# Kernel tuning notes

Hardware: AMD Instinct MI355X
Metric: run time of the kernel (lower is better)

The kernel has to match this reference:

```python
import jax, jax.numpy as jnp
import numpy as np

ROPE_BASE = 10000.0


def _rope(x):
    # Faithful to the torch module: positions indexed by x.shape[2],
    # which after split_heads is the HEADS axis. x: [B, S, H, D]
    B, S, H, D = x.shape
    theta = 1.0 / (ROPE_BASE ** (jnp.arange(0, D, 2, dtype=x.dtype) / D))  # [D/2]
    pos = jnp.arange(H, dtype=x.dtype)[:, None]  # [H, 1]
    ang = pos * theta  # [H, D/2], broadcasts against [B, S, H, D/2]
    sin, cos = jnp.sin(ang), jnp.cos(ang)
    xe, xo = x[..., 0::2], x[..., 1::2]
    re = xe * cos - xo * sin
    ro = xe * sin + xo * cos
    # interleave back: even slots <- re, odd slots <- ro
    return jnp.stack([re, ro], axis=-1).reshape(B, S, H, D)


def setup_inputs() -> dict:
    key = jax.random.key(0)
    k0, k1, k2, k3 = jax.random.split(key, 4)
    B, S, Dm = 8, 2048, 2048
    scale = 1.0 / np.sqrt(Dm)
    return {
        "x": jax.random.normal(k0, (B, S, Dm), dtype=jnp.float32),
        "Wq": jax.random.normal(k1, (Dm, Dm), dtype=jnp.float32) * scale,
        "Wk": jax.random.normal(k2, (Dm, Dm), dtype=jnp.float32) * scale,
        "Wv": jax.random.normal(k3, (Dm, Dm), dtype=jnp.float32) * scale,
        "st_pos": 0,
    }


def reference(x, Wq, Wk, Wv, st_pos):
    B, S, Dm = x.shape
    H = 16
    D = Dm // H  # head_dim = 128
    q = jnp.einsum("bsd,df->bsf", x, Wq).reshape(B, S, H, D)
    k = jnp.einsum("bsd,df->bsf", x, Wk).reshape(B, S, H, D)
    v = jnp.einsum("bsd,df->bsf", x, Wv).reshape(B, S, H, D)
    q = _rope(q)
    k = _rope(k)
    return q, k, v
```

## Files before the change

kernel.cpp:

```cpp
#include <hip/hip_runtime.h>
#include <hip/hip_bf16.h>
#include <stdint.h>


typedef __attribute__((ext_vector_type(8))) short short8;
typedef __attribute__((ext_vector_type(4))) float f32x4;

__device__ __forceinline__ unsigned short f2bf(float f) {
  __bf16 h = (__bf16)f;
  return __builtin_bit_cast(unsigned short, h);
}

__device__ __forceinline__ void gload_lds16(const void* g, void* l) {
  __builtin_amdgcn_global_load_lds((const __attribute__((address_space(1))) void*)g,
                                   (__attribute__((address_space(3))) void*)l,
                                   16, 0, 0);
}


__global__ __launch_bounds__(256) void convert_x(const float* __restrict__ X,
                                                 unsigned short* __restrict__ Xb,
                                                 int n8) {
  const int stride = gridDim.x * blockDim.x;
  for (int i = blockIdx.x * blockDim.x + threadIdx.x; i < n8; i += stride) {
    const float4 v0 = ((const float4*)X)[(size_t)i * 2 + 0];
    const float4 v1 = ((const float4*)X)[(size_t)i * 2 + 1];
    uint4 w;
    w.x = (uint32_t)f2bf(v0.x) | ((uint32_t)f2bf(v0.y) << 16);
    w.y = (uint32_t)f2bf(v0.z) | ((uint32_t)f2bf(v0.w) << 16);
    w.z = (uint32_t)f2bf(v1.x) | ((uint32_t)f2bf(v1.y) << 16);
    w.w = (uint32_t)f2bf(v1.z) | ((uint32_t)f2bf(v1.w) << 16);
    ((uint4*)Xb)[i] = w;
  }
}

__global__ __launch_bounds__(256) void transpose_cvt(const float* __restrict__ W,
                                                     unsigned short* __restrict__ WT) {
  __shared__ unsigned short tile[64][65];
  const int bx = blockIdx.x * 64;
  const int by = blockIdx.y * 64;
  const int t  = threadIdx.x;
  const int tr = t >> 4;
  const int tc = (t & 15) * 4;
#pragma unroll
  for (int i = 0; i < 4; ++i) {
    const int r = tr + i * 16;
    const float4 v = *(const float4*)&W[(size_t)(by + r) * 2048 + bx + tc];
    tile[r][tc + 0] = f2bf(v.x);
    tile[r][tc + 1] = f2bf(v.y);
    tile[r][tc + 2] = f2bf(v.z);
    tile[r][tc + 3] = f2bf(v.w);
  }
  __syncthreads();
#pragma unroll
  for (int i = 0; i < 4; ++i) {
    const int a = tr + i * 16;
    ushort4 o;
    o.x = tile[tc + 0][a];
    o.y = tile[tc + 1][a];
    o.z = tile[tc + 2][a];
    o.w = tile[tc + 3][a];
    *(ushort4*)&WT[(size_t)(bx + a) * 2048 + by + tc] = o;
  }
}


__global__ __launch_bounds__(512, 2) void qkv_fused10(const unsigned short* __restrict__ Xb,
                                                      const unsigned short* __restrict__ WT,
                                                      float* __restrict__ Out) {
  extern __shared__ char smem[];

  const int wg  = blockIdx.x;
  const int swz = (wg & 7) * 192 + (wg >> 3);
  const int mb  = swz / 24, nb = swz % 24;
  const int m0  = mb * 256, n0 = nb * 256;

  const int tid  = threadIdx.x;
  const int wave = tid >> 6, lane = tid & 63;
  const int l15  = lane & 15, lg = lane >> 4;
  const int wm   = (wave >> 2) * 128;
  const int wn   = (wave & 3) * 64;
  const int s0   = ((lg ^ (l15 & 7)) << 4);

  const unsigned short* Xp = Xb + (size_t)m0 * 2048;
  const unsigned short* Wp = WT + (size_t)n0 * 2048;

  const int srow  = tid >> 3;
  const int sslot = tid & 7;

  f32x4 acc[8][4] = {};

#define GLD_A(TP1, H)                                                         \
  do {                                                                        \
    char* dst_ = smem + (((TP1) & 1) << 16) + ((H) << 14);                    \
    _Pragma("unroll") for (int i_ = 0; i_ < 2; ++i_) {                        \
      const int row_ = (H) * 128 + i_ * 64 + srow;                            \
      gload_lds16(Xp + (size_t)row_ * 2048 + (TP1) * 64 +                     \
                      ((sslot ^ (row_ & 7)) << 3),                            \
                  dst_ + i_ * 8192 + tid * 16);                               \
    }                                                                         \
  } while (0)

#define GLD_B(TP2, H)                                                         \
  do {                                                                        \
    char* dst_ = smem + (((TP2) & 1) << 16) + 32768 + ((H) << 14);            \
    _Pragma("unroll") for (int i_ = 0; i_ < 2; ++i_) {                        \
      const int row_ = (H) * 128 + i_ * 64 + srow;                            \
      gload_lds16(Wp + (size_t)row_ * 2048 + (TP2) * 64 +                     \
                      ((sslot ^ (row_ & 7)) << 3),                            \
                  dst_ + i_ * 8192 + tid * 16);                               \
    }                                                                         \
  } while (0)

#define LDA4(MH, KS)                                                          \
  _Pragma("unroll") for (int mi_ = 0; mi_ < 4; ++mi_)                         \
      af[mi_] = *(const short8*)(Ab + ((wm + (MH) * 64 + mi_ * 16 + l15) << 7)\
                                  + (s0 ^ ((KS) << 6)));

#define PHASE_SYNC                                                            \
  __builtin_amdgcn_s_barrier();                                               \
  asm volatile("s_waitcnt lgkmcnt(0)" ::: "memory");                          \
  __builtin_amdgcn_sched_barrier(0);

#define MFMA16(MH, KS)                                                        \
  do {                                                                        \
    __builtin_amdgcn_s_setprio(1);                                            \
    _Pragma("unroll") for (int mi_ = 0; mi_ < 4; ++mi_)                       \
      _Pragma("unroll") for (int ni_ = 0; ni_ < 4; ++ni_)                     \
        asm("v_mfma_f32_16x16x32_bf16 %0, %1, %2, %0"                         \
            : "+v"(acc[(MH) * 4 + mi_][ni_])                                  \
            : "v"(af[mi_]), "v"(bfr[ni_][KS]));                               \
    __builtin_amdgcn_s_setprio(0);                                            \
  } while (0)

  GLD_A(0, 0); GLD_A(0, 1);
  GLD_B(0, 0); GLD_B(0, 1);
  GLD_B(1, 0); GLD_B(1, 1);
  asm volatile("s_waitcnt vmcnt(4)" ::: "memory");
  __builtin_amdgcn_s_barrier();

  for (int t = 0; t < 32; ++t) {
    const char* Ab = smem + ((t & 1) << 16);
    const char* Bb = Ab + 32768;
    short8 bfr[4][2], af[4];

#pragma unroll
    for (int ni_ = 0; ni_ < 4; ++ni_) {
      const char* p_ = Bb + ((wn + ni_ * 16 + l15) << 7);
      bfr[ni_][0] = *(const short8*)(p_ + s0);
      bfr[ni_][1] = *(const short8*)(p_ + (s0 ^ 64));
    }
    LDA4(0, 0);
    if (t < 31) GLD_A(t + 1, 0);
    PHASE_SYNC;
    MFMA16(0, 0);
    __builtin_amdgcn_s_barrier();

    LDA4(1, 0);
    if (t < 31) GLD_A(t + 1, 1);
    PHASE_SYNC;
    MFMA16(1, 0);
    __builtin_amdgcn_s_barrier();

    LDA4(0, 1);
    if (t < 30) GLD_B(t + 2, 0);
    PHASE_SYNC;
    MFMA16(0, 1);
    __builtin_amdgcn_s_barrier();

    LDA4(1, 1);
    if (t < 30) GLD_B(t + 2, 1);
    PHASE_SYNC;
    MFMA16(1, 1);
    if (t == 30)     asm volatile("s_waitcnt vmcnt(0)" ::: "memory");
    else if (t < 30) asm volatile("s_waitcnt vmcnt(4)" ::: "memory");
    __builtin_amdgcn_s_barrier();
  }

#undef GLD_A
#undef GLD_B
#undef LDA4
#undef PHASE_SYNC
#undef MFMA16

#pragma unroll
  for (int ni = 0; ni < 4; ++ni) {
    const int col = n0 + wn + ni * 16 + l15;
    const int sec = col >> 11;
    const int lc  = col & 2047;
    float c = 1.0f, ssg = 0.0f;
    if (sec < 2) {
      const int h = lc >> 7;
      const int p = (lc & 127) >> 1;
      const float theta = exp2f(-(float)p * 0.20762050593046014f);
      float s;
      sincosf((float)h * theta, &s, &c);
      ssg = (l15 & 1) ? s : -s;
    }
    float* outp = Out + (size_t)sec * 33554432 + lc;
#pragma unroll
    for (int mi = 0; mi < 8; ++mi) {
      const f32x4 a = acc[mi][ni];
#pragma unroll
      for (int r = 0; r < 4; ++r) {
        const float val = a[r];
        float res = val;
        if (sec < 2) {
          const float other = __shfl_xor(val, 1);
          res = val * c + other * ssg;
        }
        __builtin_nontemporal_store(
            res, outp + (size_t)(m0 + wm + mi * 16 + lg * 4 + r) * 2048);
      }
    }
  }
}

__global__ __launch_bounds__(256) void qkv_gemm_small(const float* __restrict__ X,
                                                      const unsigned short* __restrict__ WTl,
                                                      float* __restrict__ Out,
                                                      const int do_rope) {
  __shared__ unsigned short As[128 * 64];
  __shared__ unsigned short Bs[128 * 64];
  const int t    = threadIdx.x;
  const int wave = t >> 6, lane = t & 63;
  const int l15  = lane & 15, lg = lane >> 4;
  const int wm   = (wave >> 1) * 64;
  const int wn   = (wave & 1) * 64;
  const int m0   = blockIdx.y * 128;
  const int n0   = blockIdx.x * 128;

  f32x4 acc[4][4] = {};

  for (int kt = 0; kt < 2048; kt += 64) {
#pragma unroll
    for (int i = 0; i < 8; ++i) {
      const int f = i * 256 + t;
      const int row = f >> 4, chunk = f & 15;
      const float4 v = *(const float4*)&X[(size_t)(m0 + row) * 2048 + kt + chunk * 4];
      const uint32_t lo = (uint32_t)f2bf(v.x) | ((uint32_t)f2bf(v.y) << 16);
      const uint32_t hi = (uint32_t)f2bf(v.z) | ((uint32_t)f2bf(v.w) << 16);
      const int slot = chunk >> 1;
      const int off  = row * 128 + (((slot ^ (row & 7)) << 4) | ((chunk & 1) << 3));
      uint2* p = (uint2*)((char*)As + off);
      p->x = lo; p->y = hi;
    }
#pragma unroll
    for (int i = 0; i < 4; ++i) {
      const int seg = i * 4 + wave;
      const int row = seg * 8 + (lane >> 3);
      const int ps  = lane & 7;
      const int ss  = ps ^ (row & 7);
      gload_lds16(WTl + (size_t)(n0 + row) * 2048 + kt + ss * 8,
                  (char*)Bs + seg * 1024 + lane * 16);
    }
    __syncthreads();
#pragma unroll
    for (int kk = 0; kk < 2; ++kk) {
      short8 afr[4], bfr[4];
#pragma unroll
      for (int mi = 0; mi < 4; ++mi) {
        const int row  = wm + mi * 16 + l15;
        const int slot = kk * 4 + lg;
        afr[mi] = *(const short8*)((const char*)As + row * 128 + ((slot ^ (row & 7)) << 4));
      }
#pragma unroll
      for (int ni = 0; ni < 4; ++ni) {
        const int row  = wn + ni * 16 + l15;
        const int slot = kk * 4 + lg;
        bfr[ni] = *(const short8*)((const char*)Bs + row * 128 + ((slot ^ (row & 7)) << 4));
      }
#pragma unroll
      for (int mi = 0; mi < 4; ++mi)
#pragma unroll
        for (int ni = 0; ni < 4; ++ni)
          asm("v_mfma_f32_16x16x32_bf16 %0, %1, %2, %0"
              : "+v"(acc[mi][ni])
              : "v"(afr[mi]), "v"(bfr[ni]));
    }
    __syncthreads();
  }

#pragma unroll
  for (int ni = 0; ni < 4; ++ni) {
    const int col = n0 + wn + ni * 16 + l15;
    float c = 1.0f, ssg = 0.0f;
    if (do_rope) {
      const int h = col >> 7;
      const int p = (col & 127) >> 1;
      const float theta = exp2f(-(float)p * 0.20762050593046014f);
      float s;
      sincosf((float)h * theta, &s, &c);
      ssg = (l15 & 1) ? s : -s;
    }
#pragma unroll
    for (int mi = 0; mi < 4; ++mi) {
      const f32x4 a = acc[mi][ni];
#pragma unroll
      for (int r = 0; r < 4; ++r) {
        const float val = a[r];
        float res = val;
        if (do_rope) {
          const float other = __shfl_xor(val, 1);
          res = val * c + other * ssg;
        }
        Out[(size_t)(m0 + wm + mi * 16 + lg * 4 + r) * 2048 + col] = res;
      }
    }
  }
}

extern "C" void kernel_launch(void* const* d_in, const int* in_sizes, int n_in,
                              void* d_out, int out_size, void* d_ws, size_t ws_size,
                              hipStream_t stream) {
  (void)in_sizes; (void)n_in; (void)out_size;
  const float* x  = (const float*)d_in[0];
  const float* Wq = (const float*)d_in[1];
  const float* Wk = (const float*)d_in[2];
  const float* Wv = (const float*)d_in[3];
  float* out = (float*)d_out;

  const size_t XB_ELEMS = 16384ull * 2048;
  const size_t WT_ELEMS = 6144ull * 2048;
  dim3 tb(256), tg(32, 32);

  if (ws_size >= (XB_ELEMS + WT_ELEMS) * sizeof(unsigned short)) {
    unsigned short* Xb  = (unsigned short*)d_ws;
    unsigned short* WTf = Xb + XB_ELEMS;
    convert_x<<<2048, 256, 0, stream>>>(x, Xb, (int)(XB_ELEMS / 8));
    transpose_cvt<<<tg, tb, 0, stream>>>(Wq, WTf);
    transpose_cvt<<<tg, tb, 0, stream>>>(Wk, WTf + 2048ull * 2048);
    transpose_cvt<<<tg, tb, 0, stream>>>(Wv, WTf + 2ull * 2048 * 2048);
    hipFuncSetAttribute((const void*)qkv_fused10,
                        hipFuncAttributeMaxDynamicSharedMemorySize, 131072);
    qkv_fused10<<<1536, 512, 131072, stream>>>(Xb, WTf, out);
  } else {
    unsigned short* WqT = (unsigned short*)d_ws;
    unsigned short* WkT = WqT + 2048ull * 2048;
    unsigned short* WvT = WkT + 2048ull * 2048;
    transpose_cvt<<<tg, tb, 0, stream>>>(Wq, WqT);
    transpose_cvt<<<tg, tb, 0, stream>>>(Wk, WkT);
    transpose_cvt<<<tg, tb, 0, stream>>>(Wv, WvT);
    dim3 gg(16, 128);
    qkv_gemm_small<<<gg, tb, 0, stream>>>(x, WqT, out,            1);
    qkv_gemm_small<<<gg, tb, 0, stream>>>(x, WkT, out + 33554432, 1);
    qkv_gemm_small<<<gg, tb, 0, stream>>>(x, WvT, out + 67108864, 0);
  }
}
```

Before: 445.0 us.

## Switch GEMM to 32x32x16 MFMA with fragment-ordered LDS layout and merge transposes

Result: slower. 492.1 us (+10.6%).

```diff
diff --git a/kernel.cpp b/kernel.cpp
--- a/kernel.cpp
+++ b/kernel.cpp
@@ -3,8 +3,9 @@
 #include <stdint.h>
 
 
-typedef __attribute__((ext_vector_type(8))) short short8;
-typedef __attribute__((ext_vector_type(4))) float f32x4;
+typedef __attribute__((ext_vector_type(8)))  short short8;
+typedef __attribute__((ext_vector_type(4)))  float f32x4;
+typedef __attribute__((ext_vector_type(16))) float f32x16;
 
 __device__ __forceinline__ unsigned short f2bf(float f) {
   __bf16 h = (__bf16)f;
@@ -34,9 +35,14 @@
   }
 }
 
-__global__ __launch_bounds__(256) void transpose_cvt(const float* __restrict__ W,
-                                                     unsigned short* __restrict__ WT) {
+__global__ __launch_bounds__(256) void transpose_cvt3(const float* __restrict__ W0,
+                                                      const float* __restrict__ W1,
+                                                      const float* __restrict__ W2,
+                                                      unsigned short* __restrict__ WT) {
   __shared__ unsigned short tile[64][65];
+  const int z = blockIdx.z;
+  const float* W = (z == 0) ? W0 : (z == 1) ? W1 : W2;
+  unsigned short* WTz = WT + (size_t)z * 2048 * 2048;
   const int bx = blockIdx.x * 64;
   const int by = blockIdx.y * 64;
   const int t  = threadIdx.x;
@@ -60,12 +66,12 @@
     o.y = tile[tc + 1][a];
     o.z = tile[tc + 2][a];
     o.w = tile[tc + 3][a];
-    *(ushort4*)&WT[(size_t)(bx + a) * 2048 + by + tc] = o;
-  }
-}
-
-
-__global__ __launch_bounds__(512, 2) void qkv_fused10(const unsigned short* __restrict__ Xb,
+    *(ushort4*)&WTz[(size_t)(bx + a) * 2048 + by + tc] = o;
+  }
+}
+
+
+__global__ __launch_bounds__(512, 2) void qkv_fused11(const unsigned short* __restrict__ Xb,
                                                       const unsigned short* __restrict__ WT,
                                                       float* __restrict__ Out) {
   extern __shared__ char smem[];
@@ -77,59 +83,60 @@
 
   const int tid  = threadIdx.x;
   const int wave = tid >> 6, lane = tid & 63;
-  const int l15  = lane & 15, lg = lane >> 4;
+  const int l31  = lane & 31;
   const int wm   = (wave >> 2) * 128;
   const int wn   = (wave & 3) * 64;
-  const int s0   = ((lg ^ (l15 & 7)) << 4);
+  const int am   = (wave >> 2) * 4;
+  const int bn   = (wave & 3) * 2;
 
   const unsigned short* Xp = Xb + (size_t)m0 * 2048;
   const unsigned short* Wp = WT + (size_t)n0 * 2048;
 
-  const int srow  = tid >> 3;
-  const int sslot = tid & 7;
-
-  f32x4 acc[8][4] = {};
-
-#define GLD_A(TP1, H)                                                         \
+  const int sg_rowb = ((tid >> 8) << 5) + (tid & 31);
+  const int sg_koff = ((tid >> 5) & 7) * 8;
+
+  f32x16 acc[4][2] = {};
+
+#define GLD_A(TP, P)                                                          \
   do {                                                                        \
-    char* dst_ = smem + (((TP1) & 1) << 16) + ((H) << 14);                    \
+    char* dst_ = smem + (((TP) & 1) << 16);                                   \
     _Pragma("unroll") for (int i_ = 0; i_ < 2; ++i_) {                        \
-      const int row_ = (H) * 128 + i_ * 64 + srow;                            \
-      gload_lds16(Xp + (size_t)row_ * 2048 + (TP1) * 64 +                     \
-                      ((sslot ^ (row_ & 7)) << 3),                            \
-                  dst_ + i_ * 8192 + tid * 16);                               \
+      const int ch_ = 2 * (P) + i_;                                           \
+      gload_lds16(Xp + (size_t)(ch_ * 64 + sg_rowb) * 2048 + (TP) * 64 +      \
+                      sg_koff,                                                \
+                  dst_ + ch_ * 8192 + tid * 16);                              \
     }                                                                         \
   } while (0)
 
-#define GLD_B(TP2, H)                                                         \
+#define GLD_B(TP, P)                                                          \
   do {                                                                        \
-    char* dst_ = smem + (((TP2) & 1) << 16) + 32768 + ((H) << 14);            \
+    char* dst_ = smem + (((TP) & 1) << 16) + 32768;                           \
     _Pragma("unroll") for (int i_ = 0; i_ < 2; ++i_) {                        \
-      const int row_ = (H) * 128 + i_ * 64 + srow;                            \
-      gload_lds16(Wp + (size_t)row_ * 2048 + (TP2) * 64 +                     \
-                      ((sslot ^ (row_ & 7)) << 3),                            \
-                  dst_ + i_ * 8192 + tid * 16);                               \
+      const int ch_ = 2 * (P) + i_;                                           \
+      gload_lds16(Wp + (size_t)(ch_ * 64 + sg_rowb) * 2048 + (TP) * 64 +      \
+                      sg_koff,                                                \
+                  dst_ + ch_ * 8192 + tid * 16);                              \
     }                                                                         \
   } while (0)
 
-#define LDA4(MH, KS)                                                          \
-  _Pragma("unroll") for (int mi_ = 0; mi_ < 4; ++mi_)                         \
-      af[mi_] = *(const short8*)(Ab + ((wm + (MH) * 64 + mi_ * 16 + l15) << 7)\
-                                  + (s0 ^ ((KS) << 6)));
+#define LDA4(KS)                                                              \
+  _Pragma("unroll") for (int m_ = 0; m_ < 4; ++m_)                            \
+      af[m_] = *(const short8*)(Ab + (am + m_) * 4096 + (KS) * 1024 +         \
+                                lane * 16);
 
 #define PHASE_SYNC                                                            \
   __builtin_amdgcn_s_barrier();                                               \
   asm volatile("s_waitcnt lgkmcnt(0)" ::: "memory");                          \
   __builtin_amdgcn_sched_barrier(0);
 
-#define MFMA16(MH, KS)                                                        \
+#define MFMA8(KS)                                                             \
   do {                                                                        \
     __builtin_amdgcn_s_setprio(1);                                            \
-    _Pragma("unroll") for (int mi_ = 0; mi_ < 4; ++mi_)                       \
-      _Pragma("unroll") for (int ni_ = 0; ni_ < 4; ++ni_)                     \
-        asm("v_mfma_f32_16x16x32_bf16 %0, %1, %2, %0"                         \
-            : "+v"(acc[(MH) * 4 + mi_][ni_])                                  \
-            : "v"(af[mi_]), "v"(bfr[ni_][KS]));                               \
+    _Pragma("unroll") for (int m_ = 0; m_ < 4; ++m_)                          \
+      _Pragma("unroll") for (int n_ = 0; n_ < 2; ++n_)                        \
+        asm("v_mfma_f32_32x32x16_bf16 %0, %1, %2, %0"                         \
+            : "+v"(acc[m_][n_])                                               \
+            : "v"(af[m_]), "v"(bfr[n_][KS]));                                 \
     __builtin_amdgcn_s_setprio(0);                                            \
   } while (0)
 
@@ -142,36 +149,36 @@
   for (int t = 0; t < 32; ++t) {
     const char* Ab = smem + ((t & 1) << 16);
     const char* Bb = Ab + 32768;
-    short8 bfr[4][2], af[4];
-
-#pragma unroll
-    for (int ni_ = 0; ni_ < 4; ++ni_) {
-      const char* p_ = Bb + ((wn + ni_ * 16 + l15) << 7);
-      bfr[ni_][0] = *(const short8*)(p_ + s0);
-      bfr[ni_][1] = *(const short8*)(p_ + (s0 ^ 64));
-    }
-    LDA4(0, 0);
+    short8 bfr[2][4], af[4];
+
+#pragma unroll
+    for (int n_ = 0; n_ < 2; ++n_)
+#pragma unroll
+      for (int ks_ = 0; ks_ < 4; ++ks_)
+        bfr[n_][ks_] = *(const short8*)(Bb + (bn + n_) * 4096 + ks_ * 1024 +
+                                        lane * 16);
+    LDA4(0);
     if (t < 31) GLD_A(t + 1, 0);
     PHASE_SYNC;
-    MFMA16(0, 0);
+    MFMA8(0);
     __builtin_amdgcn_s_barrier();
 
-    LDA4(1, 0);
+    LDA4(1);
     if (t < 31) GLD_A(t + 1, 1);
     PHASE_SYNC;
-    MFMA16(1, 0);
+    MFMA8(1);
     __builtin_amdgcn_s_barrier();
 
-    LDA4(0, 1);
+    LDA4(2);
     if (t < 30) GLD_B(t + 2, 0);
     PHASE_SYNC;
-    MFMA16(0, 1);
+    MFMA8(2);
     __builtin_amdgcn_s_barrier();
 
-    LDA4(1, 1);
+    LDA4(3);
     if (t < 30) GLD_B(t + 2, 1);
     PHASE_SYNC;
-    MFMA16(1, 1);
+    MFMA8(3);
     if (t == 30)     asm volatile("s_waitcnt vmcnt(0)" ::: "memory");
     else if (t < 30) asm volatile("s_waitcnt vmcnt(4)" ::: "memory");
     __builtin_amdgcn_s_barrier();
@@ -181,11 +188,11 @@
 #undef GLD_B
 #undef LDA4
 #undef PHASE_SYNC
-#undef MFMA16
-
-#pragma unroll
-  for (int ni = 0; ni < 4; ++ni) {
-    const int col = n0 + wn + ni * 16 + l15;
+#undef MFMA8
+
+#pragma unroll
+  for (int n_ = 0; n_ < 2; ++n_) {
+    const int col = n0 + wn + n_ * 32 + l31;
     const int sec = col >> 11;
     const int lc  = col & 2047;
     float c = 1.0f, ssg = 0.0f;
@@ -195,22 +202,23 @@
       const float theta = exp2f(-(float)p * 0.20762050593046014f);
       float s;
       sincosf((float)h * theta, &s, &c);
-      ssg = (l15 & 1) ? s : -s;
+      ssg = (l31 & 1) ? s : -s;
     }
     float* outp = Out + (size_t)sec * 33554432 + lc;
-#pragma unroll
-    for (int mi = 0; mi < 8; ++mi) {
-      const f32x4 a = acc[mi][ni];
-#pragma unroll
-      for (int r = 0; r < 4; ++r) {
+    const int rbase = m0 + wm + 4 * (lane >> 5);
+#pragma unroll
+    for (int m_ = 0; m_ < 4; ++m_) {
+      const f32x16 a = acc[m_][n_];
+#pragma unroll
+      for (int r = 0; r < 16; ++r) {
+        const int row = rbase + m_ * 32 + (r & 3) + 8 * (r >> 2);
         const float val = a[r];
         float res = val;
         if (sec < 2) {
           const float other = __shfl_xor(val, 1);
           res = val * c + other * ssg;
         }
-        __builtin_nontemporal_store(
-            res, outp + (size_t)(m0 + wm + mi * 16 + lg * 4 + r) * 2048);
+        __builtin_nontemporal_store(res, outp + (size_t)row * 2048);
       }
     }
   }
@@ -322,25 +330,23 @@
 
   const size_t XB_ELEMS = 16384ull * 2048;
   const size_t WT_ELEMS = 6144ull * 2048;
-  dim3 tb(256), tg(32, 32);
 
   if (ws_size >= (XB_ELEMS + WT_ELEMS) * sizeof(unsigned short)) {
     unsigned short* Xb  = (unsigned short*)d_ws;
     unsigned short* WTf = Xb + XB_ELEMS;
     convert_x<<<2048, 256, 0, stream>>>(x, Xb, (int)(XB_ELEMS / 8));
-    transpose_cvt<<<tg, tb, 0, stream>>>(Wq, WTf);
-    transpose_cvt<<<tg, tb, 0, stream>>>(Wk, WTf + 2048ull * 2048);
-    transpose_cvt<<<tg, tb, 0, stream>>>(Wv, WTf + 2ull * 2048 * 2048);
-    hipFuncSetAttribute((const void*)qkv_fused10,
+    transpose_cvt3<<<dim3(32, 32, 3), 256, 0, stream>>>(Wq, Wk, Wv, WTf);
+    hipFuncSetAttribute((const void*)qkv_fused11,
                         hipFuncAttributeMaxDynamicSharedMemorySize, 131072);
-    qkv_fused10<<<1536, 512, 131072, stream>>>(Xb, WTf, out);
+    qkv_fused11<<<1536, 512, 131072, stream>>>(Xb, WTf, out);
   } else {
     unsigned short* WqT = (unsigned short*)d_ws;
     unsigned short* WkT = WqT + 2048ull * 2048;
     unsigned short* WvT = WkT + 2048ull * 2048;
-    transpose_cvt<<<tg, tb, 0, stream>>>(Wq, WqT);
-    transpose_cvt<<<tg, tb, 0, stream>>>(Wk, WkT);
-    transpose_cvt<<<tg, tb, 0, stream>>>(Wv, WvT);
+    dim3 tb(256), tg(32, 32);
+    transpose_cvt3<<<dim3(32, 32, 1), 256, 0, stream>>>(Wq, Wq, Wq, WqT);
+    transpose_cvt3<<<dim3(32, 32, 1), 256, 0, stream>>>(Wk, Wk, Wk, WkT);
+    transpose_cvt3<<<dim3(32, 32, 1), 256, 0, stream>>>(Wv, Wv, Wv, WvT);
     dim3 gg(16, 128);
     qkv_gemm_small<<<gg, tb, 0, stream>>>(x, WqT, out,            1);
     qkv_gemm_small<<<gg, tb, 0, stream>>>(x, WkT, out + 33554432, 1);
```

## Cut per-phase barriers in GEMM main loop and batch weight transposes

Applied to the files above, without the earlier changes.

After: 436.3 us. No clear change (-2.0%).

```diff
diff --git a/kernel.cpp b/kernel.cpp
--- a/kernel.cpp
+++ b/kernel.cpp
@@ -34,9 +34,14 @@
   }
 }
 
-__global__ __launch_bounds__(256) void transpose_cvt(const float* __restrict__ W,
-                                                     unsigned short* __restrict__ WT) {
+__global__ __launch_bounds__(256) void transpose_cvt3(const float* __restrict__ W0,
+                                                      const float* __restrict__ W1,
+                                                      const float* __restrict__ W2,
+                                                      unsigned short* __restrict__ WT) {
   __shared__ unsigned short tile[64][65];
+  const int z = blockIdx.z;
+  const float* W = (z == 0) ? W0 : (z == 1) ? W1 : W2;
+  unsigned short* WTz = WT + (size_t)z * 2048 * 2048;
   const int bx = blockIdx.x * 64;
   const int by = blockIdx.y * 64;
   const int t  = threadIdx.x;
@@ -60,12 +65,12 @@
     o.y = tile[tc + 1][a];
     o.z = tile[tc + 2][a];
     o.w = tile[tc + 3][a];
-    *(ushort4*)&WT[(size_t)(bx + a) * 2048 + by + tc] = o;
-  }
-}
-
-
-__global__ __launch_bounds__(512, 2) void qkv_fused10(const unsigned short* __restrict__ Xb,
+    *(ushort4*)&WTz[(size_t)(bx + a) * 2048 + by + tc] = o;
+  }
+}
+
+
+__global__ __launch_bounds__(512, 2) void qkv_fused13(const unsigned short* __restrict__ Xb,
                                                       const unsigned short* __restrict__ WT,
                                                       float* __restrict__ Out) {
   extern __shared__ char smem[];
@@ -112,24 +117,24 @@
     }                                                                         \
   } while (0)
 
-#define LDA4(MH, KS)                                                          \
+#define LDA4(DST, MH, KS)                                                     \
   _Pragma("unroll") for (int mi_ = 0; mi_ < 4; ++mi_)                         \
-      af[mi_] = *(const short8*)(Ab + ((wm + (MH) * 64 + mi_ * 16 + l15) << 7)\
-                                  + (s0 ^ ((KS) << 6)));
-
-#define PHASE_SYNC                                                            \
-  __builtin_amdgcn_s_barrier();                                               \
-  asm volatile("s_waitcnt lgkmcnt(0)" ::: "memory");                          \
-  __builtin_amdgcn_sched_barrier(0);
-
-#define MFMA16(MH, KS)                                                        \
+      (DST)[mi_] = *(const short8*)(Ab +                                      \
+          ((wm + (MH) * 64 + mi_ * 16 + l15) << 7) + (s0 ^ ((KS) << 6)));
+
+#define LDB4(DST, KS)                                                         \
+  _Pragma("unroll") for (int ni_ = 0; ni_ < 4; ++ni_)                         \
+      (DST)[ni_] = *(const short8*)(Bb +                                      \
+          ((wn + ni_ * 16 + l15) << 7) + (s0 ^ ((KS) << 6)));
+
+#define MFMA16(MH, AR, BR)                                                    \
   do {                                                                        \
     __builtin_amdgcn_s_setprio(1);                                            \
     _Pragma("unroll") for (int mi_ = 0; mi_ < 4; ++mi_)                       \
       _Pragma("unroll") for (int ni_ = 0; ni_ < 4; ++ni_)                     \
         asm("v_mfma_f32_16x16x32_bf16 %0, %1, %2, %0"                         \
             : "+v"(acc[(MH) * 4 + mi_][ni_])                                  \
-            : "v"(af[mi_]), "v"(bfr[ni_][KS]));                               \
+            : "v"((AR)[mi_]), "v"((BR)[ni_]));                                \
     __builtin_amdgcn_s_setprio(0);                                            \
   } while (0)
 
@@ -142,36 +147,24 @@
   for (int t = 0; t < 32; ++t) {
     const char* Ab = smem + ((t & 1) << 16);
     const char* Bb = Ab + 32768;
-    short8 bfr[4][2], af[4];
-
-#pragma unroll
-    for (int ni_ = 0; ni_ < 4; ++ni_) {
-      const char* p_ = Bb + ((wn + ni_ * 16 + l15) << 7);
-      bfr[ni_][0] = *(const short8*)(p_ + s0);
-      bfr[ni_][1] = *(const short8*)(p_ + (s0 ^ 64));
-    }
-    LDA4(0, 0);
+    short8 a0[4], a1[4], b0[4], b1[4];
+
+    LDB4(b0, 0);
+    LDB4(b1, 1);
+    LDA4(a0, 0, 0);
+    asm volatile("s_waitcnt lgkmcnt(0)" ::: "memory");
+    __builtin_amdgcn_s_barrier();
+    LDA4(a1, 1, 0);
     if (t < 31) GLD_A(t + 1, 0);
-    PHASE_SYNC;
-    MFMA16(0, 0);
-    __builtin_amdgcn_s_barrier();
-
-    LDA4(1, 0);
+    MFMA16(0, a0, b0);
+    LDA4(a0, 0, 1);
     if (t < 31) GLD_A(t + 1, 1);
-    PHASE_SYNC;
-    MFMA16(1, 0);
-    __builtin_amdgcn_s_barrier();
-
-    LDA4(0, 1);
+    MFMA16(1, a1, b0);
+    LDA4(a1, 1, 1);
     if (t < 30) GLD_B(t + 2, 0);
-    PHASE_SYNC;
-    MFMA16(0, 1);
-    __builtin_amdgcn_s_barrier();
-
-    LDA4(1, 1);
+    MFMA16(0, a0, b1);
     if (t < 30) GLD_B(t + 2, 1);
-    PHASE_SYNC;
-    MFMA16(1, 1);
+    MFMA16(1, a1, b1);
     if (t == 30)     asm volatile("s_waitcnt vmcnt(0)" ::: "memory");
     else if (t < 30) asm volatile("s_waitcnt vmcnt(4)" ::: "memory");
     __builtin_amdgcn_s_barrier();
@@ -180,7 +173,7 @@
 #undef GLD_A
 #undef GLD_B
 #undef LDA4
-#undef PHASE_SYNC
+#undef LDB4
 #undef MFMA16
 
 #pragma unroll
@@ -322,25 +315,23 @@
 
   const size_t XB_ELEMS = 16384ull * 2048;
   const size_t WT_ELEMS = 6144ull * 2048;
-  dim3 tb(256), tg(32, 32);
 
   if (ws_size >= (XB_ELEMS + WT_ELEMS) * sizeof(unsigned short)) {
     unsigned short* Xb  = (unsigned short*)d_ws;
     unsigned short* WTf = Xb + XB_ELEMS;
     convert_x<<<2048, 256, 0, stream>>>(x, Xb, (int)(XB_ELEMS / 8));
-    transpose_cvt<<<tg, tb, 0, stream>>>(Wq, WTf);
-    transpose_cvt<<<tg, tb, 0, stream>>>(Wk, WTf + 2048ull * 2048);
-    transpose_cvt<<<tg, tb, 0, stream>>>(Wv, WTf + 2ull * 2048 * 2048);
-    hipFuncSetAttribute((const void*)qkv_fused10,
+    transpose_cvt3<<<dim3(32, 32, 3), 256, 0, stream>>>(Wq, Wk, Wv, WTf);
+    hipFuncSetAttribute((const void*)qkv_fused13,
                         hipFuncAttributeMaxDynamicSharedMemorySize, 131072);
-    qkv_fused10<<<1536, 512, 131072, stream>>>(Xb, WTf, out);
+    qkv_fused13<<<1536, 512, 131072, stream>>>(Xb, WTf, out);
   } else {
     unsigned short* WqT = (unsigned short*)d_ws;
     unsigned short* WkT = WqT + 2048ull * 2048;
     unsigned short* WvT = WkT + 2048ull * 2048;
-    transpose_cvt<<<tg, tb, 0, stream>>>(Wq, WqT);
-    transpose_cvt<<<tg, tb, 0, stream>>>(Wk, WkT);
-    transpose_cvt<<<tg, tb, 0, stream>>>(Wv, WvT);
+    dim3 tb(256), tg(32, 32);
+    transpose_cvt3<<<dim3(32, 32, 1), 256, 0, stream>>>(Wq, Wq, Wq, WqT);
+    transpose_cvt3<<<dim3(32, 32, 1), 256, 0, stream>>>(Wk, Wk, Wk, WkT);
+    transpose_cvt3<<<dim3(32, 32, 1), 256, 0, stream>>>(Wv, Wv, Wv, WvT);
     dim3 gg(16, 128);
     qkv_gemm_small<<<gg, tb, 0, stream>>>(x, WqT, out,            1);
     qkv_gemm_small<<<gg, tb, 0, stream>>>(x, WkT, out + 33554432, 1);
```
